# Kernel optimization log

Hardware: AMD Instinct MI355X
Metric: run time of the kernel (lower is better)

The kernel has to match this reference:

```python
import jax, jax.numpy as jnp
import numpy as np

B, N, M = 2, 2048, 128
H, D = 16, 64
IN_DIM, CTX_DIM = 1024, 768


def layernorm(x, g, b, eps=1e-5):
    mu = x.mean(-1, keepdims=True)
    var = ((x - mu) ** 2).mean(-1, keepdims=True)
    return (x - mu) * jax.lax.rsqrt(var + eps) * g + b


def setup_inputs() -> dict:
    key = jax.random.key(0)
    ks = jax.random.split(key, 8)
    w = lambda i, sh: jax.random.normal(ks[i], sh, jnp.float32) * 0.02
    return {
        "x": jax.random.normal(ks[0], (B, N, IN_DIM), jnp.float32),
        "c_emb": jax.random.normal(ks[1], (B, M, CTX_DIM), jnp.float32),
        "ln_g": jnp.ones((IN_DIM,), jnp.float32),
        "ln_b": jnp.zeros((IN_DIM,), jnp.float32),
        "ctx_ln_g": jnp.ones((CTX_DIM,), jnp.float32),
        "ctx_ln_b": jnp.zeros((CTX_DIM,), jnp.float32),
        "W_ctx": w(2, (CTX_DIM, 2 * D)),
        "b_ctx": jnp.zeros((2 * D,), jnp.float32),
        "W_q": w(3, (IN_DIM, H * D)),
        "W_kv": w(4, (IN_DIM, 2 * H * D)),
        "null_kv": jax.random.normal(ks[5], (2, D), jnp.float32),
        "W_out": w(6, (H * D, IN_DIM)),
        "out_ln_g": jnp.ones((IN_DIM,), jnp.float32),
        "out_ln_b": jnp.zeros((IN_DIM,), jnp.float32),
    }


def reference(x, c_emb, ln_g, ln_b, ctx_ln_g, ctx_ln_b, W_ctx, b_ctx,
              W_q, W_kv, null_kv, W_out, out_ln_g, out_ln_b):
    b, n, _ = x.shape
    xn = layernorm(x, ln_g, ln_b)
    q = (xn @ W_q).reshape(b, n, H, D)                      # [b,n,h,d]
    kv = (xn @ W_kv).reshape(b, n, 2, H, D)
    k, v = kv[:, :, 0], kv[:, :, 1]                         # [b,n,h,d]
    # context projected to a single shared-across-heads k and v
    ckv = layernorm(c_emb, ctx_ln_g, ctx_ln_b) @ W_ctx + b_ctx
    ck, cv = jnp.split(ckv, 2, axis=-1)                     # [b,m,d]
    nk = jnp.broadcast_to(null_kv[0], (b, 1, D))
    nv = jnp.broadcast_to(null_kv[1], (b, 1, D))
    k_ext = jnp.concatenate([nk, ck], axis=1)               # [b,m+1,d]
    v_ext = jnp.concatenate([nv, cv], axis=1)
    scale = D ** -0.5
    s_self = jnp.einsum('bnhd,bkhd->bhnk', q, k) * scale    # [b,h,n,n]
    s_ctx = jnp.einsum('bnhd,bkd->bhnk', q, k_ext) * scale  # [b,h,n,m+1]
    w = jax.nn.softmax(jnp.concatenate([s_self, s_ctx], axis=-1), axis=-1)
    w_self, w_ctx = w[..., :n], w[..., n:]
    out = (jnp.einsum('bhnk,bkhd->bnhd', w_self, v)
           + jnp.einsum('bhnk,bkd->bnhd', w_ctx, v_ext))    # [b,n,h,d]
    out = out.reshape(b, n, H * D) @ W_out                  # [b,n,input_dim]
    return layernorm(out, out_ln_g, out_ln_b)
```

## Files before the change

### kernel.cpp

```cpp
#include <hip/hip_runtime.h>
#include <cstdint>
#include <cstddef>

typedef __attribute__((ext_vector_type(8))) short bf16x8;
typedef __attribute__((ext_vector_type(4))) short bf16x4;
typedef __attribute__((ext_vector_type(4))) float f32x4;
typedef __attribute__((ext_vector_type(4))) unsigned int u32x4;
typedef __attribute__((ext_vector_type(2))) unsigned int u32x2;

__device__ inline unsigned short f2b(float f){
  unsigned int u = __float_as_uint(f);
  u += 0x7fffu + ((u >> 16) & 1u);
  return (unsigned short)(u >> 16);
}
__device__ inline unsigned int pk2(float a, float b){
  unsigned int ua = __float_as_uint(a) + 0x8000u;
  unsigned int ub = __float_as_uint(b) + 0x8000u;
  return __builtin_amdgcn_perm(ub, ua, 0x07060302u);
}
__device__ inline void gl2lds16(const void* g, void* l){
  __builtin_amdgcn_global_load_lds(
      (const __attribute__((address_space(1))) unsigned int*)g,
      (__attribute__((address_space(3))) unsigned int*)l, 16, 0, 0);
}

#define QSCALE 0.18033688011112042f

__global__ __launch_bounds__(256) void wcvt_kernel(
    const float* __restrict__ Wq, const float* __restrict__ Wkv,
    const float* __restrict__ Wout,
    unsigned short* __restrict__ Wqkv_t, unsigned short* __restrict__ Wout_t)
{
  __shared__ short tile[64*72];
  int cg0 = blockIdx.x * 64;
  int kt  = blockIdx.y * 64;
  const float* src; int ld; int col0; unsigned short* dst; int drow0;
  if (cg0 < 1024)      { src = Wq;   ld = 1024; col0 = cg0;        dst = Wqkv_t; drow0 = cg0; }
  else if (cg0 < 3072) { src = Wkv;  ld = 2048; col0 = cg0 - 1024; dst = Wqkv_t; drow0 = cg0; }
  else                 { src = Wout; ld = 1024; col0 = cg0 - 3072; dst = Wout_t; drow0 = cg0 - 3072; }
  int t = threadIdx.x;
  #pragma unroll
  for (int i = 0; i < 16; ++i){
    int lin = t + 256*i;
    int k = lin >> 6, c = lin & 63;
    tile[k*72 + c] = (short)f2b(src[(size_t)(kt + k)*ld + col0 + c]);
  }
  __syncthreads();
  #pragma unroll
  for (int i = 0; i < 16; ++i){
    int lin = t + 256*i;
    int c = lin >> 6, k = lin & 63;
    dst[(size_t)(drow0 + c)*1024 + kt + k] = (unsigned short)tile[k*72 + c];
  }
}

template<bool BF16OUT>
__global__ __launch_bounds__(256) void ln1024_kernel(
    const float* __restrict__ X, const float* __restrict__ G,
    const float* __restrict__ Bb, void* __restrict__ out)
{
  int row = blockIdx.x, t = threadIdx.x;
  float4 x = ((const float4*)(X + (size_t)row*1024))[t];
  float s  = x.x + x.y + x.z + x.w;
  float s2 = x.x*x.x + x.y*x.y + x.z*x.z + x.w*x.w;
  #pragma unroll
  for (int o = 32; o > 0; o >>= 1){ s += __shfl_down(s, o); s2 += __shfl_down(s2, o); }
  __shared__ float red[8];
  int w = t >> 6;
  if ((t & 63) == 0){ red[w] = s; red[4 + w] = s2; }
  __syncthreads();
  float mu  = (red[0]+red[1]+red[2]+red[3]) * (1.0f/1024.0f);
  float var = (red[4]+red[5]+red[6]+red[7]) * (1.0f/1024.0f) - mu*mu;
  float rstd = rsqrtf(var + 1e-5f);
  float4 g = ((const float4*)G)[t];
  float4 b = ((const float4*)Bb)[t];
  float y0 = (x.x-mu)*rstd*g.x + b.x;
  float y1 = (x.y-mu)*rstd*g.y + b.y;
  float y2 = (x.z-mu)*rstd*g.z + b.z;
  float y3 = (x.w-mu)*rstd*g.w + b.w;
  if (BF16OUT){
    ushort4 u; u.x = f2b(y0); u.y = f2b(y1); u.z = f2b(y2); u.w = f2b(y3);
    ((ushort4*)out)[(size_t)row*256 + t] = u;
  } else {
    float4 y; y.x = y0; y.y = y1; y.z = y2; y.w = y3;
    ((float4*)out)[(size_t)row*256 + t] = y;
  }
}

__global__ __launch_bounds__(128) void ctx_kernel(
    const float* __restrict__ Cemb, const float* __restrict__ G,
    const float* __restrict__ Bb, const float* __restrict__ Wctx,
    const float* __restrict__ bctx, const float* __restrict__ nullkv,
    unsigned short* __restrict__ kext, unsigned short* __restrict__ vext_t)
{
  int row = blockIdx.x;
  int b = row >> 7, m = row & 127;
  int t = threadIdx.x;
  if (row < 128){
    int b2 = row >> 6, fr = row & 63;
    int frow = (fr == 0) ? 0 : (128 + fr);
    if (t < 64){
      kext[((size_t)b2*192 + frow)*64 + t] = (frow == 0) ? f2b(nullkv[t]) : (unsigned short)0;
    } else {
      int d = t - 64;
      vext_t[((size_t)b2*64 + d)*192 + frow] = (frow == 0) ? f2b(nullkv[64 + d]) : (unsigned short)0;
    }
  }
  const float* xr = Cemb + (size_t)row*768;
  float v[6]; float s = 0.f, s2 = 0.f;
  #pragma unroll
  for (int j = 0; j < 6; ++j){ float xv = xr[t + 128*j]; v[j] = xv; s += xv; s2 += xv*xv; }
  #pragma unroll
  for (int o = 32; o > 0; o >>= 1){ s += __shfl_down(s, o); s2 += __shfl_down(s2, o); }
  __shared__ float red[4];
  __shared__ float xn[768];
  int w = t >> 6;
  if ((t & 63) == 0){ red[w] = s; red[2 + w] = s2; }
  __syncthreads();
  float mu  = (red[0]+red[1]) * (1.0f/768.0f);
  float var = (red[2]+red[3]) * (1.0f/768.0f) - mu*mu;
  float rstd = rsqrtf(var + 1e-5f);
  #pragma unroll
  for (int j = 0; j < 6; ++j){ int c = t + 128*j; xn[c] = (v[j]-mu)*rstd*G[c] + Bb[c]; }
  __syncthreads();
  float acc = bctx[t];
  #pragma unroll 8
  for (int j = 0; j < 768; ++j) acc += xn[j] * Wctx[j*128 + t];
  unsigned short hv = f2b(acc);
  if (t < 64) kext[((size_t)b*192 + 1 + m)*64 + t] = hv;
  else        vext_t[((size_t)b*64 + (t - 64))*192 + 1 + m] = hv;
}

#define GEMM_MAINLOOP(A_, Bt_, tM_, tN_)                                        \
  __shared__ __align__(16) short sA[128*64];                                    \
  __shared__ __align__(16) short sB[128*64];                                    \
  int t = threadIdx.x, w = t >> 6, lane = t & 63;                               \
  int wm = w & 1, wn = w >> 1, lm = lane & 15, q = lane >> 4;                   \
  int grow = lane >> 3;                                                         \
  int gchk = ((lane & 7) ^ grow) << 3;                                          \
  f32x4 acc[4][4] = {};                                                         \
  const unsigned short* Aw = A_ + (size_t)(tM_ + w*32 + grow)*1024 + gchk;      \
  const unsigned short* Bw = Bt_ + (size_t)(tN_ + w*32 + grow)*1024 + gchk;     \
  for (int kk = 0; kk < 1024; kk += 64){                                        \
    __syncthreads();                                                            \
    gl2lds16(Aw + kk,            &sA[(w*32     )*64]);                          \
    gl2lds16(Aw + kk +  8*1024,  &sA[(w*32 +  8)*64]);                          \
    gl2lds16(Aw + kk + 16*1024,  &sA[(w*32 + 16)*64]);                          \
    gl2lds16(Aw + kk + 24*1024,  &sA[(w*32 + 24)*64]);                          \
    gl2lds16(Bw + kk,            &sB[(w*32     )*64]);                          \
    gl2lds16(Bw + kk +  8*1024,  &sB[(w*32 +  8)*64]);                          \
    gl2lds16(Bw + kk + 16*1024,  &sB[(w*32 + 16)*64]);                          \
    gl2lds16(Bw + kk + 24*1024,  &sB[(w*32 + 24)*64]);                          \
    __syncthreads();                                                            \
    bf16x8 af[4][2], bfr[4][2];                                                 \
    _Pragma("unroll")                                                           \
    for (int i = 0; i < 4; ++i){                                                \
      int ra = wm*64 + i*16 + lm, rb = wn*64 + i*16 + lm;                       \
      _Pragma("unroll")                                                         \
      for (int hh = 0; hh < 2; ++hh){                                           \
        int sw = ((hh*4 + q) ^ (lm & 7)) << 3;                                  \
        af[i][hh]  = *(const bf16x8*)(&sA[ra*64 + sw]);                         \
        bfr[i][hh] = *(const bf16x8*)(&sB[rb*64 + sw]);                         \
      }                                                                         \
    }                                                                           \
    _Pragma("unroll")                                                           \
    for (int hh = 0; hh < 2; ++hh)                                              \
      _Pragma("unroll")                                                         \
      for (int i = 0; i < 4; ++i)                                               \
        _Pragma("unroll")                                                       \
        for (int j = 0; j < 4; ++j)                                             \
          acc[i][j] = __builtin_amdgcn_mfma_f32_16x16x32_bf16(af[i][hh], bfr[j][hh], acc[i][j], 0, 0, 0); \
  }

__global__ __launch_bounds__(256) void gemm_qkv_kernel(
    const unsigned short* __restrict__ A, const unsigned short* __restrict__ Bt,
    unsigned short* __restrict__ Qb, unsigned short* __restrict__ Kb,
    unsigned short* __restrict__ VtG)
{
  int id = blockIdx.x;
  int xcd = id & 7, r = id >> 3;
  int tM = ((r & 3)*8 + xcd) * 128;
  int tN = (r >> 2) * 128;
  GEMM_MAINLOOP(A, Bt, tM, tN)
  if (tN < 1024){
    #pragma unroll
    for (int i = 0; i < 4; ++i){
      int R0 = tM + wm*64 + i*16 + q*4;
      int b = R0 >> 11, n = R0 & 2047;
      #pragma unroll
      for (int j = 0; j < 4; ++j){
        int Cg = tN + wn*64 + j*16 + lm;
        int h = Cg >> 6, d = Cg & 63;
        size_t base = ((((size_t)(b*16 + h) << 11) | n) << 6) + d;
        #pragma unroll
        for (int rr = 0; rr < 4; ++rr)
          Qb[base + (size_t)rr*64] = f2b(acc[i][j][rr] * QSCALE);
      }
    }
  } else if (tN < 2048){
    #pragma unroll
    for (int i = 0; i < 4; ++i){
      int R0 = tM + wm*64 + i*16 + q*4;
      int b = R0 >> 11, n = R0 & 2047;
      #pragma unroll
      for (int j = 0; j < 4; ++j){
        int c2 = tN - 1024 + wn*64 + j*16 + lm;
        int h = c2 >> 6, d = c2 & 63;
        size_t base = ((((size_t)(b*16 + h) << 11) | n) << 6) + d;
        #pragma unroll
        for (int rr = 0; rr < 4; ++rr)
          Kb[base + (size_t)rr*64] = f2b(acc[i][j][rr]);
      }
    }
  } else {
    #pragma unroll
    for (int i = 0; i < 4; ++i){
      int R0 = tM + wm*64 + i*16 + q*4;
      int b = R0 >> 11, n = R0 & 2047;
      #pragma unroll
      for (int j = 0; j < 4; ++j){
        int c2 = tN - 2048 + wn*64 + j*16 + lm;
        int h = c2 >> 6, d = c2 & 63;
        ushort4 u;
        u.x = f2b(acc[i][j][0]); u.y = f2b(acc[i][j][1]);
        u.z = f2b(acc[i][j][2]); u.w = f2b(acc[i][j][3]);
        *(ushort4*)(VtG + ((size_t)(b*16 + h)*64 + d)*2048 + n) = u;
      }
    }
  }
}

__global__ __launch_bounds__(256) void gemm_out_kernel(
    const unsigned short* __restrict__ A, const unsigned short* __restrict__ Bt,
    float* __restrict__ C)
{
  int id = blockIdx.x;
  int xcd = id & 7, r = id >> 3;
  int tM = ((r & 3)*8 + xcd) * 128;
  int tN = (r >> 2) * 128;
  GEMM_MAINLOOP(A, Bt, tM, tN)
  #pragma unroll
  for (int i = 0; i < 4; ++i){
    int R0 = tM + wm*64 + i*16 + q*4;
    #pragma unroll
    for (int j = 0; j < 4; ++j){
      int Cg = tN + wn*64 + j*16 + lm;
      #pragma unroll
      for (int rr = 0; rr < 4; ++rr)
        C[(size_t)(R0 + rr)*1024 + Cg] = acc[i][j][rr];
    }
  }
}

__global__ __launch_bounds__(256, 2) void attn_kernel(
    const unsigned short* __restrict__ Qb, const unsigned short* __restrict__ Kb,
    const unsigned short* __restrict__ VtG, const unsigned short* __restrict__ kext,
    const unsigned short* __restrict__ vext_t, unsigned short* __restrict__ Ob)
{
  __shared__ __align__(16) char smem[54272];
  int id = blockIdx.x;
  int xcd = id & 7, slot = id >> 3;
  int bh = xcd*4 + (slot >> 4);
  int qt = slot & 15;
  int b = bh >> 4, h = bh & 15;
  int t = threadIdx.x, w = t >> 6, lane = t & 63;
  int p = w >> 1, lw = w & 1;
  int lm = lane & 15, q = lane >> 4;

  short* myK = (short*)(smem + p*9216);
  short* myV = (short*)(smem + 18432 + p*9216);
  short* pw  = (short*)(smem + 36864 + w*4352);

  const unsigned short* Qbase = Qb + ((size_t)bh*2048 + qt*128 + lw*64)*64;
  bf16x8 qf[4][2];
  #pragma unroll
  for (int qq = 0; qq < 4; ++qq){
    qf[qq][0] = *(const bf16x8*)(Qbase + (size_t)(qq*16 + lm)*64 + q*8);
    qf[qq][1] = *(const bf16x8*)(Qbase + (size_t)(qq*16 + lm)*64 + q*8 + 32);
  }

  f32x4 o[4][4] = {};
  float l_i[4] = {0.f, 0.f, 0.f, 0.f};

  int pt = t & 127;
  int r0 = pt >> 1, c0 = (pt & 1) << 5;
  const int t0 = p ? 18 : 0;
  const int t1 = p ? 35 : 18;

  u32x4 kr[4], vr[4];
  {
    const unsigned short* kp = Kb + ((size_t)bh*2048 + t0*64 + r0)*64 + c0;
    const unsigned short* vp = VtG + ((size_t)bh*64 + r0)*2048 + t0*64 + c0;
    #pragma unroll
    for (int jj = 0; jj < 4; ++jj){
      kr[jj] = *(const u32x4*)(kp + 8*jj);
      vr[jj] = *(const u32x4*)(vp + 8*jj);
    }
  }

  for (int it = 0; it < 18; ++it){
    int tile = t0 + it;
    bool valid = tile < t1;
    __syncthreads();
    if (valid){
      #pragma unroll
      for (int jj = 0; jj < 4; ++jj){
        *(u32x4*)(&myK[r0*72 + c0 + 8*jj]) = kr[jj];
        *(u32x4*)(&myV[r0*72 + c0 + 8*jj]) = vr[jj];
      }
    }
    __syncthreads();

    int nt = tile + 1;
    if (nt < t1){
      bool ext = nt >= 32;
      int kb = ext ? (nt - 32)*64 : nt*64;
      const unsigned short* kp = ext ? (kext + ((size_t)b*192 + kb + r0)*64 + c0)
                                     : (Kb + ((size_t)bh*2048 + kb + r0)*64 + c0);
      const unsigned short* vp = ext ? (vext_t + ((size_t)b*64 + r0)*192 + kb + c0)
                                     : (VtG + ((size_t)bh*64 + r0)*2048 + kb + c0);
      #pragma unroll
      for (int jj = 0; jj < 4; ++jj){
        kr[jj] = *(const u32x4*)(kp + 8*jj);
        vr[jj] = *(const u32x4*)(vp + 8*jj);
      }
    }
    if (!valid) continue;

    bf16x8 kf[4][2];
    #pragma unroll
    for (int st = 0; st < 4; ++st){
      kf[st][0] = *(const bf16x8*)(&myK[(st*16 + lm)*72 + q*8]);
      kf[st][1] = *(const bf16x8*)(&myK[(st*16 + lm)*72 + q*8 + 32]);
    }

    #pragma unroll
    for (int qp = 0; qp < 2; ++qp){
      f32x4 s[2][4];
      #pragma unroll
      for (int qh = 0; qh < 2; ++qh){
        int qq = qp*2 + qh;
        #pragma unroll
        for (int st = 0; st < 4; ++st){
          f32x4 z = {};
          z = __builtin_amdgcn_mfma_f32_16x16x32_bf16(kf[st][0], qf[qq][0], z, 0, 0, 0);
          s[qh][st] = __builtin_amdgcn_mfma_f32_16x16x32_bf16(kf[st][1], qf[qq][1], z, 0, 0, 0);
        }
      }
      if (tile == 34){
        #pragma unroll
        for (int qh = 0; qh < 2; ++qh)
          #pragma unroll
          for (int st = 0; st < 4; ++st)
            #pragma unroll
            for (int rr = 0; rr < 4; ++rr){
              int key = 128 + st*16 + q*4 + rr;
              if (key >= 129) s[qh][st][rr] = -1e30f;
            }
      }
      #pragma unroll
      for (int qh = 0; qh < 2; ++qh){
        float sm = 0.f;
        #pragma unroll
        for (int st = 0; st < 4; ++st)
          #pragma unroll
          for (int rr = 0; rr < 4; ++rr){
            float pv = __builtin_amdgcn_exp2f(s[qh][st][rr]);
            s[qh][st][rr] = pv; sm += pv;
          }
        l_i[qp*2 + qh] += sm;
        #pragma unroll
        for (int st = 0; st < 4; ++st){
          u32x2 pkd;
          pkd[0] = pk2(s[qh][st][0], s[qh][st][1]);
          pkd[1] = pk2(s[qh][st][2], s[qh][st][3]);
          *(u32x2*)(&pw[(qh*16 + lm)*68 + st*16 + q*4]) = pkd;
        }
      }
      bf16x8 pb[2][2];
      #pragma unroll
      for (int qh = 0; qh < 2; ++qh){
        bf16x4 a0 = *(const bf16x4*)(&pw[(qh*16 + lm)*68 + q*8]);
        bf16x4 a1 = *(const bf16x4*)(&pw[(qh*16 + lm)*68 + q*8 + 4]);
        bf16x4 a2 = *(const bf16x4*)(&pw[(qh*16 + lm)*68 + 32 + q*8]);
        bf16x4 a3 = *(const bf16x4*)(&pw[(qh*16 + lm)*68 + 32 + q*8 + 4]);
        pb[qh][0] = __builtin_shufflevector(a0, a1, 0,1,2,3,4,5,6,7);
        pb[qh][1] = __builtin_shufflevector(a2, a3, 0,1,2,3,4,5,6,7);
      }
      #pragma unroll
      for (int ds = 0; ds < 4; ++ds){
        bf16x8 af0 = *(const bf16x8*)(&myV[(ds*16 + lm)*72 + q*8]);
        bf16x8 af1 = *(const bf16x8*)(&myV[(ds*16 + lm)*72 + q*8 + 32]);
        #pragma unroll
        for (int qh = 0; qh < 2; ++qh){
          int qq = qp*2 + qh;
          o[ds][qq] = __builtin_amdgcn_mfma_f32_16x16x32_bf16(af0, pb[qh][0], o[ds][qq], 0, 0, 0);
          o[ds][qq] = __builtin_amdgcn_mfma_f32_16x16x32_bf16(af1, pb[qh][1], o[ds][qq], 0, 0, 0);
        }
      }
    }
  }

  float* mb = (float*)smem;
  float* reg = mb + lw*4352 + lane*68;
  __syncthreads();
  if (p == 1){
    #pragma unroll
    for (int ds = 0; ds < 4; ++ds)
      #pragma unroll
      for (int qq = 0; qq < 4; ++qq)
        *(f32x4*)(reg + (ds*4 + qq)*4) = o[ds][qq];
    #pragma unroll
    for (int qq = 0; qq < 4; ++qq) reg[64 + qq] = l_i[qq];
  }
  __syncthreads();
  if (p == 0){
    #pragma unroll
    for (int qq = 0; qq < 4; ++qq){
      #pragma unroll
      for (int ds = 0; ds < 4; ++ds){
        f32x4 ov = *(const f32x4*)(reg + (ds*4 + qq)*4);
        o[ds][qq] += ov;
      }
      float l = l_i[qq] + reg[64 + qq];
      l += __shfl_xor(l, 16);
      l += __shfl_xor(l, 32);
      float inv = 1.0f / l;
      int n = qt*128 + lw*64 + qq*16 + lm;
      size_t base = ((size_t)b*2048 + n)*1024 + h*64 + q*4;
      #pragma unroll
      for (int ds = 0; ds < 4; ++ds){
        ushort4 u;
        u.x = f2b(o[ds][qq][0] * inv); u.y = f2b(o[ds][qq][1] * inv);
        u.z = f2b(o[ds][qq][2] * inv); u.w = f2b(o[ds][qq][3] * inv);
        *(ushort4*)(Ob + base + ds*16) = u;
      }
    }
  }
}

extern "C" void kernel_launch(void* const* d_in, const int* in_sizes, int n_in,
                              void* d_out, int out_size, void* d_ws, size_t ws_size,
                              hipStream_t stream)
{
  const float* x       = (const float*)d_in[0];
  const float* c_emb   = (const float*)d_in[1];
  const float* ln_g    = (const float*)d_in[2];
  const float* ln_b    = (const float*)d_in[3];
  const float* ctx_g   = (const float*)d_in[4];
  const float* ctx_b   = (const float*)d_in[5];
  const float* W_ctx   = (const float*)d_in[6];
  const float* b_ctx   = (const float*)d_in[7];
  const float* W_q     = (const float*)d_in[8];
  const float* W_kv    = (const float*)d_in[9];
  const float* null_kv = (const float*)d_in[10];
  const float* W_out   = (const float*)d_in[11];
  const float* oln_g   = (const float*)d_in[12];
  const float* oln_b   = (const float*)d_in[13];
  float* out = (float*)d_out;

  char* p = (char*)d_ws;
  unsigned short* xn     = (unsigned short*)p; p += (size_t)4096*1024*2;
  unsigned short* Wqkv_t = (unsigned short*)p; p += (size_t)3072*1024*2;
  unsigned short* Wout_t = (unsigned short*)p; p += (size_t)1024*1024*2;
  unsigned short* Qb     = (unsigned short*)p; p += (size_t)32*2048*64*2;
  unsigned short* Kb     = (unsigned short*)p; p += (size_t)32*2048*64*2;
  unsigned short* VtG    = (unsigned short*)p; p += (size_t)32*64*2048*2;
  unsigned short* kext   = (unsigned short*)p; p += (size_t)2*192*64*2;
  unsigned short* vext_t = (unsigned short*)p; p += (size_t)2*64*192*2;
  unsigned short* aout   = (unsigned short*)p; p += (size_t)4096*1024*2;
  float*          ptmp   = (float*)p;          p += (size_t)4096*1024*4;

  wcvt_kernel<<<dim3(64,16), 256, 0, stream>>>(W_q, W_kv, W_out, Wqkv_t, Wout_t);
  ln1024_kernel<true><<<4096, 256, 0, stream>>>(x, ln_g, ln_b, (void*)xn);
  ctx_kernel<<<256, 128, 0, stream>>>(c_emb, ctx_g, ctx_b, W_ctx, b_ctx, null_kv, kext, vext_t);
  gemm_qkv_kernel<<<768, 256, 0, stream>>>(xn, Wqkv_t, Qb, Kb, VtG);
  attn_kernel<<<512, 256, 0, stream>>>(Qb, Kb, VtG, kext, vext_t, aout);
  gemm_out_kernel<<<256, 256, 0, stream>>>(aout, Wout_t, ptmp);
  ln1024_kernel<false><<<4096, 256, 0, stream>>>(ptmp, oln_g, oln_b, (void*)out);
}
```

Baseline: 275.4 us.

## Split attention key range four ways per block with XOR-swizzled LDS tiles

The attention kernel now launches 512 threads per block, with four wave-pairs each handling about a quarter of the key tiles instead of two halves. Each pair loops over 9 tiles instead of 18, and the partial outputs and row sums are merged in a two-level tree through shared memory. The K, V and P LDS buffers drop the padded row stride in favour of XOR swizzling, which aims to avoid bank conflicts without padding. Shared memory per block grows to 80 KB, and the extra reduction steps and barriers may limit how many blocks fit on each CU.

```diff
diff --git a/kernel.cpp b/kernel.cpp
--- a/kernel.cpp
+++ b/kernel.cpp
@@ -252,12 +252,12 @@
   }
 }
 
-__global__ __launch_bounds__(256, 2) void attn_kernel(
+__global__ __launch_bounds__(512, 4) void attn_kernel(
     const unsigned short* __restrict__ Qb, const unsigned short* __restrict__ Kb,
     const unsigned short* __restrict__ VtG, const unsigned short* __restrict__ kext,
     const unsigned short* __restrict__ vext_t, unsigned short* __restrict__ Ob)
 {
-  __shared__ __align__(16) char smem[54272];
+  __shared__ __align__(16) char smem[81920];
   int id = blockIdx.x;
   int xcd = id & 7, slot = id >> 3;
   int bh = xcd*4 + (slot >> 4);
@@ -266,10 +266,11 @@
   int t = threadIdx.x, w = t >> 6, lane = t & 63;
   int p = w >> 1, lw = w & 1;
   int lm = lane & 15, q = lane >> 4;
-
-  short* myK = (short*)(smem + p*9216);
-  short* myV = (short*)(smem + 18432 + p*9216);
-  short* pw  = (short*)(smem + 36864 + w*4352);
+  int esw = lm & 7;
+
+  short* myK = (short*)(smem + p*8192);
+  short* myV = (short*)(smem + 32768 + p*8192);
+  short* pw  = (short*)(smem + 65536 + w*2048);
 
   const unsigned short* Qbase = Qb + ((size_t)bh*2048 + qt*128 + lw*64)*64;
   bf16x8 qf[4][2];
@@ -284,8 +285,9 @@
 
   int pt = t & 127;
   int r0 = pt >> 1, c0 = (pt & 1) << 5;
-  const int t0 = p ? 18 : 0;
-  const int t1 = p ? 35 : 18;
+  int rsw = r0 & 7;
+  const int t0 = p*9;
+  const int t1 = (p == 3) ? 35 : (t0 + 9);
 
   u32x4 kr[4], vr[4];
   {
@@ -298,15 +300,16 @@
     }
   }
 
-  for (int it = 0; it < 18; ++it){
+  for (int it = 0; it < 9; ++it){
     int tile = t0 + it;
     bool valid = tile < t1;
     __syncthreads();
     if (valid){
       #pragma unroll
       for (int jj = 0; jj < 4; ++jj){
-        *(u32x4*)(&myK[r0*72 + c0 + 8*jj]) = kr[jj];
-        *(u32x4*)(&myV[r0*72 + c0 + 8*jj]) = vr[jj];
+        int gsw = ((((pt & 1) << 2) | jj) ^ rsw) << 3;
+        *(u32x4*)(&myK[r0*64 + gsw]) = kr[jj];
+        *(u32x4*)(&myV[r0*64 + gsw]) = vr[jj];
       }
     }
     __syncthreads();
@@ -330,8 +333,8 @@
     bf16x8 kf[4][2];
     #pragma unroll
     for (int st = 0; st < 4; ++st){
-      kf[st][0] = *(const bf16x8*)(&myK[(st*16 + lm)*72 + q*8]);
-      kf[st][1] = *(const bf16x8*)(&myK[(st*16 + lm)*72 + q*8 + 32]);
+      kf[st][0] = *(const bf16x8*)(&myK[(st*16 + lm)*64 + ((q       ^ esw) << 3)]);
+      kf[st][1] = *(const bf16x8*)(&myK[(st*16 + lm)*64 + (((4 + q) ^ esw) << 3)]);
     }
 
     #pragma unroll
@@ -358,6 +361,7 @@
               if (key >= 129) s[qh][st][rr] = -1e30f;
             }
       }
+      bf16x8 pb[2][2];
       #pragma unroll
       for (int qh = 0; qh < 2; ++qh){
         float sm = 0.f;
@@ -374,23 +378,20 @@
           u32x2 pkd;
           pkd[0] = pk2(s[qh][st][0], s[qh][st][1]);
           pkd[1] = pk2(s[qh][st][2], s[qh][st][3]);
-          *(u32x2*)(&pw[(qh*16 + lm)*68 + st*16 + q*4]) = pkd;
+          int gsw = ((((st << 1) | (q >> 1)) ^ esw) << 3) + ((q & 1) << 2);
+          *(u32x2*)(&pw[lm*64 + gsw]) = pkd;
         }
-      }
-      bf16x8 pb[2][2];
-      #pragma unroll
-      for (int qh = 0; qh < 2; ++qh){
-        bf16x4 a0 = *(const bf16x4*)(&pw[(qh*16 + lm)*68 + q*8]);
-        bf16x4 a1 = *(const bf16x4*)(&pw[(qh*16 + lm)*68 + q*8 + 4]);
-        bf16x4 a2 = *(const bf16x4*)(&pw[(qh*16 + lm)*68 + 32 + q*8]);
-        bf16x4 a3 = *(const bf16x4*)(&pw[(qh*16 + lm)*68 + 32 + q*8 + 4]);
+        bf16x4 a0 = *(const bf16x4*)(&pw[lm*64 + ((q       ^ esw) << 3)]);
+        bf16x4 a1 = *(const bf16x4*)(&pw[lm*64 + ((q       ^ esw) << 3) + 4]);
+        bf16x4 a2 = *(const bf16x4*)(&pw[lm*64 + (((4 + q) ^ esw) << 3)]);
+        bf16x4 a3 = *(const bf16x4*)(&pw[lm*64 + (((4 + q) ^ esw) << 3) + 4]);
         pb[qh][0] = __builtin_shufflevector(a0, a1, 0,1,2,3,4,5,6,7);
         pb[qh][1] = __builtin_shufflevector(a2, a3, 0,1,2,3,4,5,6,7);
       }
       #pragma unroll
       for (int ds = 0; ds < 4; ++ds){
-        bf16x8 af0 = *(const bf16x8*)(&myV[(ds*16 + lm)*72 + q*8]);
-        bf16x8 af1 = *(const bf16x8*)(&myV[(ds*16 + lm)*72 + q*8 + 32]);
+        bf16x8 af0 = *(const bf16x8*)(&myV[(ds*16 + lm)*64 + ((q       ^ esw) << 3)]);
+        bf16x8 af1 = *(const bf16x8*)(&myV[(ds*16 + lm)*64 + (((4 + q) ^ esw) << 3)]);
         #pragma unroll
         for (int qh = 0; qh < 2; ++qh){
           int qq = qp*2 + qh;
@@ -402,27 +403,52 @@
   }
 
   float* mb = (float*)smem;
-  float* reg = mb + lw*4352 + lane*68;
-  __syncthreads();
-  if (p == 1){
+  float* lb = (float*)(smem + 65536);
+  int ms = ((p >> 1) << 1) | lw;
+  float* reg = mb + ms*4096 + lane*64;
+  float* lr  = lb + ms*256 + lane*4;
+  int fsw = lane & 15;
+  __syncthreads();
+  if (p & 1){
     #pragma unroll
     for (int ds = 0; ds < 4; ++ds)
       #pragma unroll
       for (int qq = 0; qq < 4; ++qq)
-        *(f32x4*)(reg + (ds*4 + qq)*4) = o[ds][qq];
-    #pragma unroll
-    for (int qq = 0; qq < 4; ++qq) reg[64 + qq] = l_i[qq];
+        *(f32x4*)(reg + (((ds*4 + qq) ^ fsw) << 2)) = o[ds][qq];
+    #pragma unroll
+    for (int qq = 0; qq < 4; ++qq) lr[qq] = l_i[qq];
+  }
+  __syncthreads();
+  if (!(p & 1)){
+    #pragma unroll
+    for (int ds = 0; ds < 4; ++ds)
+      #pragma unroll
+      for (int qq = 0; qq < 4; ++qq)
+        o[ds][qq] += *(const f32x4*)(reg + (((ds*4 + qq) ^ fsw) << 2));
+    #pragma unroll
+    for (int qq = 0; qq < 4; ++qq) l_i[qq] += lr[qq];
+    if (p == 2){
+      #pragma unroll
+      for (int ds = 0; ds < 4; ++ds)
+        #pragma unroll
+        for (int qq = 0; qq < 4; ++qq)
+          *(f32x4*)(reg + (((ds*4 + qq) ^ fsw) << 2)) = o[ds][qq];
+      #pragma unroll
+      for (int qq = 0; qq < 4; ++qq) lr[qq] = l_i[qq];
+    }
   }
   __syncthreads();
   if (p == 0){
+    float* reg2 = mb + (2 | lw)*4096 + lane*64;
+    float* lr2  = lb + (2 | lw)*256 + lane*4;
     #pragma unroll
     for (int qq = 0; qq < 4; ++qq){
       #pragma unroll
       for (int ds = 0; ds < 4; ++ds){
-        f32x4 ov = *(const f32x4*)(reg + (ds*4 + qq)*4);
+        f32x4 ov = *(const f32x4*)(reg2 + (((ds*4 + qq) ^ fsw) << 2));
         o[ds][qq] += ov;
       }
-      float l = l_i[qq] + reg[64 + qq];
+      float l = l_i[qq] + lr2[qq];
       l += __shfl_xor(l, 16);
       l += __shfl_xor(l, 32);
       float inv = 1.0f / l;
@@ -475,7 +501,7 @@
   ln1024_kernel<true><<<4096, 256, 0, stream>>>(x, ln_g, ln_b, (void*)xn);
   ctx_kernel<<<256, 128, 0, stream>>>(c_emb, ctx_g, ctx_b, W_ctx, b_ctx, null_kv, kext, vext_t);
   gemm_qkv_kernel<<<768, 256, 0, stream>>>(xn, Wqkv_t, Qb, Kb, VtG);
-  attn_kernel<<<512, 256, 0, stream>>>(Qb, Kb, VtG, kext, vext_t, aout);
+  attn_kernel<<<512, 512, 0, stream>>>(Qb, Kb, VtG, kext, vext_t, aout);
   gemm_out_kernel<<<256, 256, 0, stream>>>(aout, Wout_t, ptmp);
   ln1024_kernel<false><<<4096, 256, 0, stream>>>(ptmp, oln_g, oln_b, (void*)out);
 }
```

Result: slower. 543.8 us (+97.4%).
